# Performance work log

Hardware: AMD Instinct MI355X
Metric: run time of the kernel (lower is better)

Reference implementation:

```python
import math
import jax, jax.numpy as jnp
import numpy as np
from jax.scipy.special import gammaln, xlogy

HEADS = 8
DIM_KEY = 64
DIM_VALUE = 64
NUM_REL_POS_FEATURES = 192
DIM = 768
SEQ = 2048
BATCH = 2


def get_positional_embed(seq_len: int, feature_size: int) -> jnp.ndarray:
    # distances: [2n-1]
    distances = jnp.arange(-seq_len + 1, seq_len, dtype=jnp.float32)
    f = feature_size // 6  # 3 basis classes, then doubled with sign term
    absd = jnp.abs(distances)[:, None]  # [2n-1, 1]
    # exponential basis
    max_range = math.log(seq_len) / math.log(2.0)
    half_life = 2.0 ** jnp.linspace(3.0, max_range, f)[None, :]
    exp_feat = jnp.exp(-math.log(2.0) / half_life * absd)
    # central mask basis
    center_widths = 2.0 ** jnp.arange(1, f + 1, dtype=jnp.float32) - 1.0
    cmask = (center_widths[None, :] > absd).astype(jnp.float32)
    # gamma pdf basis
    stddev = seq_len / (2.0 * f)
    start_mean = seq_len / f
    mean = jnp.linspace(start_mean, float(seq_len), f)[None, :]
    concentration = (mean / stddev) ** 2
    rate = mean / stddev ** 2
    log_unnorm = xlogy(concentration - 1.0, absd) - rate * absd
    log_norm = gammaln(concentration) - concentration * jnp.log(rate)
    probs = jnp.exp(log_unnorm - log_norm) + 1e-8
    gamma_feat = probs / jnp.max(probs, axis=-1, keepdims=True)
    emb = jnp.concatenate([exp_feat, cmask, gamma_feat], axis=-1)  # [2n-1, 3f]
    return jnp.concatenate([emb, jnp.sign(distances)[:, None] * emb], axis=-1)  # [2n-1, 6f]


def relative_shift(x: jnp.ndarray) -> jnp.ndarray:
    # x: [b, h, n, 2n-1] -> [b, h, n, n] via Transformer-XL shift trick
    x = jnp.concatenate([jnp.zeros_like(x[..., :1]), x], axis=-1)
    b, h, t1, t2 = x.shape  # t2 = 2n
    x = x.reshape(b, h, t2, t1)[:, :, 1:, :].reshape(b, h, t1, t2 - 1)
    return x[..., : (t2 + 1) // 2]


def setup_inputs() -> dict:
    key = jax.random.key(0)
    ks = jax.random.split(key, 9)
    d_inner = HEADS * DIM_KEY
    d_vinner = HEADS * DIM_VALUE
    sc = 1.0 / math.sqrt(DIM)
    return {
        "x": jax.random.normal(ks[0], (BATCH, SEQ, DIM), dtype=jnp.float32),
        "Wq": jax.random.normal(ks[1], (DIM, d_inner), dtype=jnp.float32) * sc,
        "Wk": jax.random.normal(ks[2], (DIM, d_inner), dtype=jnp.float32) * sc,
        "Wv": jax.random.normal(ks[3], (DIM, d_vinner), dtype=jnp.float32) * sc,
        "Wrel": jax.random.normal(ks[4], (NUM_REL_POS_FEATURES, d_inner), dtype=jnp.float32) * (1.0 / math.sqrt(NUM_REL_POS_FEATURES)),
        "rel_content_bias": jax.random.normal(ks[5], (1, HEADS, 1, DIM_KEY), dtype=jnp.float32),
        "rel_pos_bias": jax.random.normal(ks[6], (1, HEADS, 1, DIM_KEY), dtype=jnp.float32),
        "Wo": jax.random.normal(ks[7], (d_vinner, DIM), dtype=jnp.float32) * (1.0 / math.sqrt(d_vinner)),
        "bo": jax.random.normal(ks[8], (DIM,), dtype=jnp.float32) * 0.01,
    }


def reference(x, Wq, Wk, Wv, Wrel, rel_content_bias, rel_pos_bias, Wo, bo):
    b, n, _ = x.shape
    scale = DIM_KEY ** -0.5
    # projections -> [b, h, n, d]
    q = (x @ Wq).reshape(b, n, HEADS, DIM_KEY).transpose(0, 2, 1, 3) * scale
    k = (x @ Wk).reshape(b, n, HEADS, DIM_KEY).transpose(0, 2, 1, 3)
    v = (x @ Wv).reshape(b, n, HEADS, DIM_VALUE).transpose(0, 2, 1, 3)
    content_logits = jnp.einsum("bhid,bhjd->bhij", q + rel_content_bias, k)
    positions = get_positional_embed(n, NUM_REL_POS_FEATURES)  # [2n-1, F]
    rel_k = (positions @ Wrel).reshape(2 * n - 1, HEADS, DIM_KEY).transpose(1, 0, 2)  # [h, 2n-1, d]
    rel_logits = jnp.einsum("bhid,hjd->bhij", q + rel_pos_bias, rel_k)
    rel_logits = relative_shift(rel_logits)  # [b, h, n, n]
    attn = jax.nn.softmax(content_logits + rel_logits, axis=-1)
    out = jnp.einsum("bhij,bhjd->bhid", attn, v)  # [b, h, n, dv]
    out = out.transpose(0, 2, 1, 3).reshape(b, n, HEADS * DIM_VALUE)
    return out @ Wo + bo
```

## Files before the change

kernel.cpp:

```cpp
#include <hip/hip_runtime.h>
#include <hip/hip_bf16.h>
#include <math.h>


typedef _Float16 f16x8 __attribute__((ext_vector_type(8)));
typedef _Float16 f16x4 __attribute__((ext_vector_type(4)));
typedef float f32x4 __attribute__((ext_vector_type(4)));

#define MFMA16(a, b, c) __builtin_amdgcn_mfma_f32_16x16x32_f16((a), (b), (c), 0, 0, 0)

__global__ __launch_bounds__(256) void cvt4_kernel(const float* __restrict__ in,
                                                   _Float16* __restrict__ out, int n4) {
  int idx = blockIdx.x * 256 + threadIdx.x;
  if (idx < n4) {
    float4 v = ((const float4*)in)[idx];
    f16x4 o;
    o[0] = (_Float16)v.x; o[1] = (_Float16)v.y; o[2] = (_Float16)v.z; o[3] = (_Float16)v.w;
    ((f16x4*)out)[idx] = o;
  }
}

__global__ __launch_bounds__(256) void cvt_t_tile_kernel(const float* __restrict__ in,
                                                         _Float16* __restrict__ out,
                                                         int K, int N) {
  __shared__ float tile[32][33];
  const int k0 = blockIdx.y * 32, n0 = blockIdx.x * 32;
  const int t = threadIdx.x;
  const int tr = t >> 3, tc = (t & 7) * 4;
  float4 v = *(const float4*)(in + (size_t)(k0 + tr) * N + n0 + tc);
  tile[tr][tc] = v.x; tile[tr][tc + 1] = v.y; tile[tr][tc + 2] = v.z; tile[tr][tc + 3] = v.w;
  __syncthreads();
  f16x4 o;
  o[0] = (_Float16)tile[tc][tr];
  o[1] = (_Float16)tile[tc + 1][tr];
  o[2] = (_Float16)tile[tc + 2][tr];
  o[3] = (_Float16)tile[tc + 3][tr];
  *(f16x4*)(out + (size_t)(n0 + tr) * K + k0 + tc) = o;
}

__global__ __launch_bounds__(256) void cvt_t3_tile_kernel(const float* __restrict__ Wq,
                                                          const float* __restrict__ Wk,
                                                          const float* __restrict__ Wv,
                                                          _Float16* __restrict__ out) {
  __shared__ float tile[32][33];
  const int z = blockIdx.z;
  const float* in = (z == 0) ? Wq : (z == 1) ? Wk : Wv;
  const int k0 = blockIdx.y * 32, n0 = blockIdx.x * 32;
  const int t = threadIdx.x;
  const int tr = t >> 3, tc = (t & 7) * 4;
  float4 v = *(const float4*)(in + (size_t)(k0 + tr) * 512 + n0 + tc);
  tile[tr][tc] = v.x; tile[tr][tc + 1] = v.y; tile[tr][tc + 2] = v.z; tile[tr][tc + 3] = v.w;
  __syncthreads();
  f16x4 o;
  o[0] = (_Float16)tile[tc][tr];
  o[1] = (_Float16)tile[tc + 1][tr];
  o[2] = (_Float16)tile[tc + 2][tr];
  o[3] = (_Float16)tile[tc + 3][tr];
  *(f16x4*)(out + ((size_t)z * 512 + n0 + tr) * 768 + k0 + tc) = o;
}

__global__ __launch_bounds__(64) void pos_const_kernel(float* __restrict__ lnrm) {
  int t = threadIdx.x;
  if (t < 32) {
    float mean = 64.f * (float)(t + 1);
    float sd = 32.f;
    float conc = (mean / sd) * (mean / sd);
    float rate = mean / (sd * sd);
    lnrm[t] = lgammaf(conc) - conc * logf(rate);
  }
}

__global__ __launch_bounds__(128) void pos_embed_kernel(_Float16* __restrict__ posb,
                                                        const float* __restrict__ lnrm) {
  const int t = threadIdx.x;
  const int lr = t >> 5, i = t & 31;
  const int r = blockIdx.x * 4 + lr;
  _Float16* row = posb + (size_t)r * 192;
  if (r >= 4095) {
    row[i] = (_Float16)0.f; row[32 + i] = (_Float16)0.f; row[64 + i] = (_Float16)0.f;
    row[96 + i] = (_Float16)0.f; row[128 + i] = (_Float16)0.f; row[160 + i] = (_Float16)0.f;
    return;
  }
  const float dist = (float)(r - 2047);
  const float absd = fabsf(dist);
  const float sgn = (dist > 0.f) ? 1.f : ((dist < 0.f) ? -1.f : 0.f);
  const float e = 3.f + (float)i * (8.f / 31.f);
  const float expv = exp2f(-absd * exp2f(-e));
  const float cw = exp2f((float)(i + 1)) - 1.f;
  const float cm = (cw > absd) ? 1.f : 0.f;
  const float mean = 64.f * (float)(i + 1);
  const float conc = (mean / 32.f) * (mean / 32.f);
  const float rate = mean / 1024.f;
  const float lu = (conc - 1.f) * logf(absd) - rate * absd;
  float gv = expf(lu - lnrm[i]) + 1e-8f;
  float mx = gv;
  mx = fmaxf(mx, __shfl_xor(mx, 1));
  mx = fmaxf(mx, __shfl_xor(mx, 2));
  mx = fmaxf(mx, __shfl_xor(mx, 4));
  mx = fmaxf(mx, __shfl_xor(mx, 8));
  mx = fmaxf(mx, __shfl_xor(mx, 16));
  gv /= mx;
  row[i] = (_Float16)expv;       row[32 + i] = (_Float16)cm;        row[64 + i] = (_Float16)gv;
  row[96 + i] = (_Float16)(sgn * expv); row[128 + i] = (_Float16)(sgn * cm); row[160 + i] = (_Float16)(sgn * gv);
}

template <int MODE>
__global__ __launch_bounds__(256, 3) void gemm_tile(
    const _Float16* __restrict__ A, const _Float16* __restrict__ Bt,
    const int N, const int K,
    _Float16* __restrict__ o0, _Float16* __restrict__ o1,
    _Float16* __restrict__ o2, _Float16* __restrict__ o3,
    const float* __restrict__ bias0, const float* __restrict__ bias1,
    float* __restrict__ outf) {
  __shared__ __align__(16) _Float16 As[2][128 * 32];
  __shared__ __align__(16) _Float16 Bs[2][128 * 32];
  const int tid = threadIdx.x;
  const int w = tid >> 6, lane = tid & 63, g = lane >> 4, m = lane & 15;
  const int wr = w >> 1, wc = w & 1;
  const int row0 = blockIdx.y * 128;
  const int c0 = blockIdx.x * 128;

  const int sr0 = tid >> 2, ssl = tid & 3;
  const _Float16* Ag = A + (size_t)(row0 + sr0) * K + ssl * 8;
  const _Float16* Bg = Bt + (size_t)(c0 + sr0) * K + ssl * 8;
  const size_t gstep = (size_t)64 * K;
  const int wo0 = sr0 * 64 + ((ssl ^ ((sr0 >> 1) & 3)) << 4);

  int aoff[4], boff[4];
#pragma unroll
  for (int i = 0; i < 4; ++i) {
    const int ar = wr * 64 + i * 16 + m;
    aoff[i] = ar * 64 + ((g ^ ((ar >> 1) & 3)) << 4);
    const int br = wc * 64 + i * 16 + m;
    boff[i] = br * 64 + ((g ^ ((br >> 1) & 3)) << 4);
  }

  f16x8 a0, a1, b0, b1;
#define GLOAD(k0v)                                      \
  a0 = *(const f16x8*)(Ag + (k0v));                     \
  a1 = *(const f16x8*)(Ag + gstep + (k0v));             \
  b0 = *(const f16x8*)(Bg + (k0v));                     \
  b1 = *(const f16x8*)(Bg + gstep + (k0v));
#define SWRITE(buf)                                     \
  *(f16x8*)((char*)As[buf] + wo0) = a0;                 \
  *(f16x8*)((char*)As[buf] + wo0 + 4096) = a1;          \
  *(f16x8*)((char*)Bs[buf] + wo0) = b0;                 \
  *(f16x8*)((char*)Bs[buf] + wo0 + 4096) = b1;

  f32x4 acc[4][4] = {};
  GLOAD(0); SWRITE(0);
  __syncthreads();
  const int nk = K >> 5;
  for (int ks = 0; ks < nk; ++ks) {
    const int cur = ks & 1;
    if (ks + 1 < nk) { GLOAD((ks + 1) << 5); }
    const char* ap = (const char*)As[cur];
    const char* bp = (const char*)Bs[cur];
    f16x8 af[4], bf[4];
#pragma unroll
    for (int i = 0; i < 4; ++i) {
      af[i] = *(const f16x8*)(ap + aoff[i]);
      bf[i] = *(const f16x8*)(bp + boff[i]);
    }
#pragma unroll
    for (int mi = 0; mi < 4; ++mi)
#pragma unroll
      for (int ni = 0; ni < 4; ++ni)
        acc[mi][ni] = MFMA16(af[mi], bf[ni], acc[mi][ni]);
    if (ks + 1 < nk) { SWRITE(cur ^ 1); }
    __syncthreads();
  }
#undef GLOAD
#undef SWRITE

  const int proj = (MODE == 0) ? (c0 >> 9) : 0;
#pragma unroll
  for (int ni = 0; ni < 4; ++ni) {
    const int col = c0 + wc * 64 + ni * 16 + m;
    const int c = col & 511, hh = (MODE == 0) ? (c >> 6) : (col >> 6);
    const int dk = col & 63;
    float b0f = 0.f, b1f = 0.f;
    if (MODE == 0 && proj == 0) { b0f = bias0[c]; b1f = bias1[c]; }
    if (MODE == 0 && proj == 2) {
#pragma unroll
      for (int mi = 0; mi < 4; ++mi) {
        const int rowb = row0 + wr * 64 + mi * 16 + g * 4;
        const int bb = rowb >> 11, n = rowb & 2047;
        f16x4 pk;
#pragma unroll
        for (int r = 0; r < 4; ++r) pk[r] = (_Float16)acc[mi][ni][r];
        *(f16x4*)(o3 + ((size_t)(bb * 8 + hh) * 64 + dk) * 2048 + n) = pk;
      }
    } else {
#pragma unroll
      for (int mi = 0; mi < 4; ++mi) {
#pragma unroll
        for (int r = 0; r < 4; ++r) {
          const int row = row0 + wr * 64 + mi * 16 + g * 4 + r;
          const float v = acc[mi][ni][r];
          if (MODE == 0) {
            const int bb = row >> 11, n = row & 2047;
            const size_t ad = ((size_t)(bb * 8 + hh) * 2048 + n) * 64 + dk;
            if (proj == 0) {
              const float vs = v * 0.125f;
              o0[ad] = (_Float16)(vs + b0f);
              o1[ad] = (_Float16)(vs + b1f);
            } else {
              o2[ad] = (_Float16)v;
            }
          } else if (MODE == 3) {
            o0[((size_t)hh * 4096 + row) * 64 + dk] = (_Float16)v;
          } else {
            outf[(size_t)row * N + col] = v + bias0[col];
          }
        }
      }
    }
  }
}

__global__ __launch_bounds__(256, 2) void attn_kernel(
    const _Float16* __restrict__ qc, const _Float16* __restrict__ qp,
    const _Float16* __restrict__ kb, const _Float16* __restrict__ vtb,
    const _Float16* __restrict__ relkb, _Float16* __restrict__ attnb) {
  __shared__ __align__(16) char lds[2 * 32768 + 4 * 2304];
  const int tid = threadIdx.x;
  const int w = tid >> 6, lane = tid & 63, g = lane >> 4, m = lane & 15;
  const int L = blockIdx.x;
  const int h = L & 7;
  const int r2 = L >> 3;
  const int b = r2 >> 5, xt = r2 & 31;
  const int bh = b * 8 + h;
  const int i0b = xt << 6;
  const int i0 = i0b + w * 16;

  const int srow = tid >> 3;
  const int ssl = tid & 7;
  const int swz = (srow << 7) + ((ssl ^ (srow & 7)) << 4);
  const char* kgb = (const char*)kb + ((size_t)bh << 18);
  const char* vgb = (const char*)vtb + ((size_t)bh << 18);
  const char* rgb = (const char*)relkb + ((size_t)h << 19);

  f16x8 ska, skb_, sva, svb, sra, srb, src_, srd;
#define STAGE_LOAD(j0v, d0v)                                                          \
  ska  = *(const f16x8*)(kgb + ((size_t)((j0v) + srow) << 7) + (ssl << 4));           \
  skb_ = *(const f16x8*)(kgb + ((size_t)((j0v) + srow + 32) << 7) + (ssl << 4));      \
  sva  = *(const f16x8*)(vgb + ((size_t)srow << 12) + ((j0v) << 1) + (ssl << 4));     \
  svb  = *(const f16x8*)(vgb + ((size_t)(srow + 32) << 12) + ((j0v) << 1) + (ssl << 4)); \
  sra  = *(const f16x8*)(rgb + ((size_t)((d0v) + srow) << 7) + (ssl << 4));           \
  srb  = *(const f16x8*)(rgb + ((size_t)((d0v) + srow + 32) << 7) + (ssl << 4));      \
  src_ = *(const f16x8*)(rgb + ((size_t)((d0v) + srow + 64) << 7) + (ssl << 4));      \
  srd  = *(const f16x8*)(rgb + ((size_t)((d0v) + srow + 96) << 7) + (ssl << 4));

#define STAGE_WRITE(halfp)                          \
  *(f16x8*)((halfp) + swz) = ska;                   \
  *(f16x8*)((halfp) + swz + 4096) = skb_;           \
  *(f16x8*)((halfp) + 8192 + swz) = sva;            \
  *(f16x8*)((halfp) + 8192 + swz + 4096) = svb;     \
  *(f16x8*)((halfp) + 16384 + swz) = sra;           \
  *(f16x8*)((halfp) + 16384 + swz + 4096) = srb;    \
  *(f16x8*)((halfp) + 16384 + swz + 8192) = src_;   \
  *(f16x8*)((halfp) + 16384 + swz + 12288) = srd;

  STAGE_LOAD(0, 1984 - i0b);
  { char* nh = lds; STAGE_WRITE(nh); }

  const size_t qbase = ((size_t)bh * 2048 + i0 + m) * 64 + g * 8;
  f16x8 qcf0 = *(const f16x8*)(qc + qbase);
  f16x8 qcf1 = *(const f16x8*)(qc + qbase + 32);
  f16x8 qpf0 = *(const f16x8*)(qp + qbase);
  f16x8 qpf1 = *(const f16x8*)(qp + qbase + 32);

  __syncthreads();

  f32x4 acc_o[4] = {};
  float m_run[4], l_run[4];
#pragma unroll
  for (int r = 0; r < 4; ++r) { m_run[r] = -1e30f; l_run[r] = 0.f; }

  const int sx = m & 7;
  const int fo0 = (g ^ sx) << 4;
  const int fo1 = ((4 | g) ^ sx) << 4;
  const int rrow0 = 48 - (w << 4) + m;
  _Float16* Pl = (_Float16*)(lds + 65536 + w * 2304);

  for (int jt = 0; jt < 32; ++jt) {
    if (jt < 31) {
      const int j0n = (jt + 1) << 6;
      STAGE_LOAD(j0n, j0n - i0b + 1984);
    }
    const char* curh = lds + ((jt & 1) << 15);
    f32x4 sc[4] = {};
#pragma unroll
    for (int cf = 0; cf < 4; ++cf) {
      const char* kp = curh + ((m + (cf << 4)) << 7);
      sc[cf] = MFMA16(qcf0, *(const f16x8*)(kp + fo0), sc[cf]);
      sc[cf] = MFMA16(qcf1, *(const f16x8*)(kp + fo1), sc[cf]);
    }
    f32x4 rc[5] = {};
#pragma unroll
    for (int cf = 0; cf < 5; ++cf) {
      const char* rp = curh + 16384 + ((rrow0 + (cf << 4)) << 7);
      rc[cf] = MFMA16(qpf0, *(const f16x8*)(rp + fo0), rc[cf]);
      rc[cf] = MFMA16(qpf1, *(const f16x8*)(rp + fo1), rc[cf]);
    }
#pragma unroll
    for (int r = 0; r < 4; ++r) {
      const int lr = g * 4 + r;
      const int u = 15 + m - lr;
      const int src = (g << 4) | (u & 15);
      const bool hi = (m > lr);
      float sh0 = __shfl(rc[0][r], src);
      float sh1 = __shfl(rc[1][r], src);
      float sh2 = __shfl(rc[2][r], src);
      float sh3 = __shfl(rc[3][r], src);
      float sh4 = __shfl(rc[4][r], src);
      sc[0][r] += hi ? sh1 : sh0;
      sc[1][r] += hi ? sh2 : sh1;
      sc[2][r] += hi ? sh3 : sh2;
      sc[3][r] += hi ? sh4 : sh3;
    }
    float P[4][4];
#pragma unroll
    for (int r = 0; r < 4; ++r) {
      float mx = fmaxf(fmaxf(sc[0][r], sc[1][r]), fmaxf(sc[2][r], sc[3][r]));
      mx = fmaxf(mx, __shfl_xor(mx, 1));
      mx = fmaxf(mx, __shfl_xor(mx, 2));
      mx = fmaxf(mx, __shfl_xor(mx, 4));
      mx = fmaxf(mx, __shfl_xor(mx, 8));
      const float mnew = fmaxf(m_run[r], mx);
      const float corr = __expf(m_run[r] - mnew);
      float rs = 0.f;
#pragma unroll
      for (int cf = 0; cf < 4; ++cf) {
        float p = __expf(sc[cf][r] - mnew);
        P[cf][r] = p;
        rs += p;
      }
      rs += __shfl_xor(rs, 1);
      rs += __shfl_xor(rs, 2);
      rs += __shfl_xor(rs, 4);
      rs += __shfl_xor(rs, 8);
      l_run[r] = l_run[r] * corr + rs;
      m_run[r] = mnew;
#pragma unroll
      for (int cf = 0; cf < 4; ++cf) acc_o[cf][r] *= corr;
    }
#pragma unroll
    for (int cf = 0; cf < 4; ++cf)
#pragma unroll
      for (int r = 0; r < 4; ++r)
        Pl[(g * 4 + r) * 72 + cf * 16 + m] = (_Float16)P[cf][r];
#pragma unroll
    for (int ks = 0; ks < 2; ++ks) {
      f16x8 pa = *(const f16x8*)((const char*)Pl + m * 144 + ks * 64 + (g << 4));
#pragma unroll
      for (int cf = 0; cf < 4; ++cf) {
        const char* vp = curh + 8192 + ((m + (cf << 4)) << 7);
        acc_o[cf] = MFMA16(pa, *(const f16x8*)(vp + (ks ? fo1 : fo0)), acc_o[cf]);
      }
    }
    if (jt < 31) {
      char* nh = lds + (((jt & 1) ^ 1) << 15);
      STAGE_WRITE(nh);
    }
    __syncthreads();
  }
#pragma unroll
  for (int cf = 0; cf < 4; ++cf)
#pragma unroll
    for (int r = 0; r < 4; ++r) {
      const int i = i0 + g * 4 + r;
      const float o = acc_o[cf][r] / l_run[r];
      attnb[((size_t)(b * 2048 + i)) * 512 + h * 64 + cf * 16 + m] = (_Float16)o;
    }
#undef STAGE_LOAD
#undef STAGE_WRITE
}

extern "C" void kernel_launch(void* const* d_in, const int* in_sizes, int n_in,
                              void* d_out, int out_size, void* d_ws, size_t ws_size,
                              hipStream_t stream) {
  (void)in_sizes; (void)n_in; (void)out_size; (void)ws_size;
  const float* x    = (const float*)d_in[0];
  const float* Wq   = (const float*)d_in[1];
  const float* Wk   = (const float*)d_in[2];
  const float* Wv   = (const float*)d_in[3];
  const float* Wrel = (const float*)d_in[4];
  const float* bc   = (const float*)d_in[5];
  const float* bp   = (const float*)d_in[6];
  const float* Wo   = (const float*)d_in[7];
  const float* bo   = (const float*)d_in[8];
  float* out = (float*)d_out;

  char* ws = (char*)d_ws;
  size_t off = 0;
  auto alloc = [&](size_t bytes) -> void* {
    void* p = ws + off;
    off += (bytes + 255) & ~(size_t)255;
    return p;
  };
  _Float16* xb     = (_Float16*)alloc(4096ull * 768 * 2);
  _Float16* wqkvt  = (_Float16*)alloc(1536ull * 768 * 2);
  _Float16* wrelt  = (_Float16*)alloc(512ull * 192 * 2);
  _Float16* wot    = (_Float16*)alloc(768ull * 512 * 2);
  _Float16* posb   = (_Float16*)alloc(4096ull * 192 * 2);
  float*    lnrm   = (float*)alloc(32 * 4);
  _Float16* qcb    = (_Float16*)alloc(16ull * 2048 * 64 * 2);
  _Float16* qpb    = (_Float16*)alloc(16ull * 2048 * 64 * 2);
  _Float16* kbb    = (_Float16*)alloc(16ull * 2048 * 64 * 2);
  _Float16* vtb    = (_Float16*)alloc(16ull * 64 * 2048 * 2);
  _Float16* relkb  = (_Float16*)alloc(8ull * 4096 * 64 * 2);
  _Float16* attnb  = (_Float16*)alloc(4096ull * 512 * 2);

  cvt4_kernel<<<3072, 256, 0, stream>>>(x, xb, 786432);
  cvt_t3_tile_kernel<<<dim3(16, 24, 3), 256, 0, stream>>>(Wq, Wk, Wv, wqkvt);
  cvt_t_tile_kernel<<<dim3(16, 6), 256, 0, stream>>>(Wrel, wrelt, 192, 512);
  cvt_t_tile_kernel<<<dim3(24, 16), 256, 0, stream>>>(Wo, wot, 512, 768);
  pos_const_kernel<<<1, 64, 0, stream>>>(lnrm);
  pos_embed_kernel<<<1024, 128, 0, stream>>>(posb, lnrm);

  gemm_tile<0><<<dim3(12, 32), 256, 0, stream>>>(xb, wqkvt, 1536, 768,
                                                 qcb, qpb, kbb, vtb, bc, bp, nullptr);
  gemm_tile<3><<<dim3(4, 32), 256, 0, stream>>>(posb, wrelt, 512, 192,
                                                relkb, nullptr, nullptr, nullptr,
                                                nullptr, nullptr, nullptr);

  attn_kernel<<<512, 256, 0, stream>>>(qcb, qpb, kbb, vtb, relkb, attnb);

  gemm_tile<4><<<dim3(6, 32), 256, 0, stream>>>(attnb, wot, 768, 512,
                                                nullptr, nullptr, nullptr, nullptr,
                                                bo, nullptr, out);
}
```

Measured before the change: 213.5 us.

## Fuse prep kernels, use direct global-to-LDS loads, shrink GEMM tiles, MFMA row sums

All conversion and positional-embedding kernels are merged into one prep launch, and the lgamma constants are computed inline. The GEMM and attention kernels now stage K/V/rel-K and GEMM operands with global_load_lds, which copies straight into shared memory without passing through registers. The swizzle moves to the global source address. GEMM tiles shrink to 64 rows with occupancy 4 and twice the grid to fill more CUs. In attention, the softmax max reduction uses DPP and the row sum is accumulated by an MFMA against a ones vector instead of shuffles, which adds some MFMA work.

```diff
diff --git a/kernel.cpp b/kernel.cpp
--- a/kernel.cpp
+++ b/kernel.cpp
@@ -9,72 +9,75 @@
 
 #define MFMA16(a, b, c) __builtin_amdgcn_mfma_f32_16x16x32_f16((a), (b), (c), 0, 0, 0)
 
-__global__ __launch_bounds__(256) void cvt4_kernel(const float* __restrict__ in,
-                                                   _Float16* __restrict__ out, int n4) {
-  int idx = blockIdx.x * 256 + threadIdx.x;
-  if (idx < n4) {
-    float4 v = ((const float4*)in)[idx];
+#define GL16(gp, lp)                                                       \
+  __builtin_amdgcn_global_load_lds(                                        \
+      (const __attribute__((address_space(1))) void*)(gp),                 \
+      (__attribute__((address_space(3))) void*)(lp), 16, 0, 0)
+
+__device__ __forceinline__ float dpp_fmax16(float x) {
+  int v;
+  v = __builtin_amdgcn_update_dpp(0, __float_as_int(x), 0xB1, 0xf, 0xf, true);
+  x = fmaxf(x, __int_as_float(v));
+  v = __builtin_amdgcn_update_dpp(0, __float_as_int(x), 0x4E, 0xf, 0xf, true);
+  x = fmaxf(x, __int_as_float(v));
+  v = __builtin_amdgcn_update_dpp(0, __float_as_int(x), 0x141, 0xf, 0xf, true);
+  x = fmaxf(x, __int_as_float(v));
+  v = __builtin_amdgcn_update_dpp(0, __float_as_int(x), 0x140, 0xf, 0xf, true);
+  x = fmaxf(x, __int_as_float(v));
+  return x;
+}
+
+__global__ __launch_bounds__(256) void prep_kernel(
+    const float* __restrict__ x, const float* __restrict__ Wq,
+    const float* __restrict__ Wk, const float* __restrict__ Wv,
+    const float* __restrict__ Wrel, const float* __restrict__ Wo,
+    _Float16* __restrict__ xb, _Float16* __restrict__ wqkvt,
+    _Float16* __restrict__ wrelt, _Float16* __restrict__ wot,
+    _Float16* __restrict__ posb) {
+  __shared__ float tile[32][33];
+  const int t = threadIdx.x;
+  int bid = blockIdx.x;
+  if (bid < 3072) {
+    const int idx = bid * 256 + t;
+    float4 v = ((const float4*)x)[idx];
     f16x4 o;
     o[0] = (_Float16)v.x; o[1] = (_Float16)v.y; o[2] = (_Float16)v.z; o[3] = (_Float16)v.w;
-    ((f16x4*)out)[idx] = o;
-  }
-}
-
-__global__ __launch_bounds__(256) void cvt_t_tile_kernel(const float* __restrict__ in,
-                                                         _Float16* __restrict__ out,
-                                                         int K, int N) {
-  __shared__ float tile[32][33];
-  const int k0 = blockIdx.y * 32, n0 = blockIdx.x * 32;
-  const int t = threadIdx.x;
-  const int tr = t >> 3, tc = (t & 7) * 4;
-  float4 v = *(const float4*)(in + (size_t)(k0 + tr) * N + n0 + tc);
-  tile[tr][tc] = v.x; tile[tr][tc + 1] = v.y; tile[tr][tc + 2] = v.z; tile[tr][tc + 3] = v.w;
-  __syncthreads();
-  f16x4 o;
-  o[0] = (_Float16)tile[tc][tr];
-  o[1] = (_Float16)tile[tc + 1][tr];
-  o[2] = (_Float16)tile[tc + 2][tr];
-  o[3] = (_Float16)tile[tc + 3][tr];
-  *(f16x4*)(out + (size_t)(n0 + tr) * K + k0 + tc) = o;
-}
-
-__global__ __launch_bounds__(256) void cvt_t3_tile_kernel(const float* __restrict__ Wq,
-                                                          const float* __restrict__ Wk,
-                                                          const float* __restrict__ Wv,
-                                                          _Float16* __restrict__ out) {
-  __shared__ float tile[32][33];
-  const int z = blockIdx.z;
-  const float* in = (z == 0) ? Wq : (z == 1) ? Wk : Wv;
-  const int k0 = blockIdx.y * 32, n0 = blockIdx.x * 32;
-  const int t = threadIdx.x;
-  const int tr = t >> 3, tc = (t & 7) * 4;
-  float4 v = *(const float4*)(in + (size_t)(k0 + tr) * 512 + n0 + tc);
-  tile[tr][tc] = v.x; tile[tr][tc + 1] = v.y; tile[tr][tc + 2] = v.z; tile[tr][tc + 3] = v.w;
-  __syncthreads();
-  f16x4 o;
-  o[0] = (_Float16)tile[tc][tr];
-  o[1] = (_Float16)tile[tc + 1][tr];
-  o[2] = (_Float16)tile[tc + 2][tr];
-  o[3] = (_Float16)tile[tc + 3][tr];
-  *(f16x4*)(out + ((size_t)z * 512 + n0 + tr) * 768 + k0 + tc) = o;
-}
-
-__global__ __launch_bounds__(64) void pos_const_kernel(float* __restrict__ lnrm) {
-  int t = threadIdx.x;
-  if (t < 32) {
-    float mean = 64.f * (float)(t + 1);
-    float sd = 32.f;
-    float conc = (mean / sd) * (mean / sd);
-    float rate = mean / (sd * sd);
-    lnrm[t] = lgammaf(conc) - conc * logf(rate);
-  }
-}
-
-__global__ __launch_bounds__(128) void pos_embed_kernel(_Float16* __restrict__ posb,
-                                                        const float* __restrict__ lnrm) {
-  const int t = threadIdx.x;
+    ((f16x4*)xb)[idx] = o;
+    return;
+  }
+  bid -= 3072;
+  if (bid < 1632) {
+    const float* in; _Float16* out; int K_, N_, bx, by;
+    if (bid < 1152) {
+      const int z = bid / 384, rem = bid % 384;
+      in = (z == 0) ? Wq : (z == 1) ? Wk : Wv;
+      out = wqkvt + (size_t)z * 512 * 768;
+      K_ = 768; N_ = 512; bx = rem & 15; by = rem >> 4;
+    } else if (bid < 1248) {
+      const int rem = bid - 1152;
+      in = Wrel; out = wrelt;
+      K_ = 192; N_ = 512; bx = rem & 15; by = rem >> 4;
+    } else {
+      const int rem = bid - 1248;
+      in = Wo; out = wot;
+      K_ = 512; N_ = 768; bx = rem % 24; by = rem / 24;
+    }
+    const int k0 = by * 32, n0 = bx * 32;
+    const int tr = t >> 3, tc = (t & 7) * 4;
+    float4 v = *(const float4*)(in + (size_t)(k0 + tr) * N_ + n0 + tc);
+    tile[tr][tc] = v.x; tile[tr][tc + 1] = v.y; tile[tr][tc + 2] = v.z; tile[tr][tc + 3] = v.w;
+    __syncthreads();
+    f16x4 o;
+    o[0] = (_Float16)tile[tc][tr];
+    o[1] = (_Float16)tile[tc + 1][tr];
+    o[2] = (_Float16)tile[tc + 2][tr];
+    o[3] = (_Float16)tile[tc + 3][tr];
+    *(f16x4*)(out + (size_t)(n0 + tr) * K_ + k0 + tc) = o;
+    return;
+  }
+  bid -= 1632;
   const int lr = t >> 5, i = t & 31;
-  const int r = blockIdx.x * 4 + lr;
+  const int r = bid * 8 + lr;
   _Float16* row = posb + (size_t)r * 192;
   if (r >= 4095) {
     row[i] = (_Float16)0.f; row[32 + i] = (_Float16)0.f; row[64 + i] = (_Float16)0.f;
@@ -91,8 +94,9 @@
   const float mean = 64.f * (float)(i + 1);
   const float conc = (mean / 32.f) * (mean / 32.f);
   const float rate = mean / 1024.f;
+  const float lnrm = lgammaf(conc) - conc * logf(rate);
   const float lu = (conc - 1.f) * logf(absd) - rate * absd;
-  float gv = expf(lu - lnrm[i]) + 1e-8f;
+  float gv = expf(lu - lnrm) + 1e-8f;
   float mx = gv;
   mx = fmaxf(mx, __shfl_xor(mx, 1));
   mx = fmaxf(mx, __shfl_xor(mx, 2));
@@ -100,78 +104,76 @@
   mx = fmaxf(mx, __shfl_xor(mx, 8));
   mx = fmaxf(mx, __shfl_xor(mx, 16));
   gv /= mx;
-  row[i] = (_Float16)expv;       row[32 + i] = (_Float16)cm;        row[64 + i] = (_Float16)gv;
-  row[96 + i] = (_Float16)(sgn * expv); row[128 + i] = (_Float16)(sgn * cm); row[160 + i] = (_Float16)(sgn * gv);
+  row[i] = (_Float16)expv;              row[32 + i] = (_Float16)cm;
+  row[64 + i] = (_Float16)gv;           row[96 + i] = (_Float16)(sgn * expv);
+  row[128 + i] = (_Float16)(sgn * cm);  row[160 + i] = (_Float16)(sgn * gv);
 }
 
 template <int MODE>
-__global__ __launch_bounds__(256, 3) void gemm_tile(
+__global__ __launch_bounds__(256, 4) void gemm_tile(
     const _Float16* __restrict__ A, const _Float16* __restrict__ Bt,
     const int N, const int K,
     _Float16* __restrict__ o0, _Float16* __restrict__ o1,
     _Float16* __restrict__ o2, _Float16* __restrict__ o3,
     const float* __restrict__ bias0, const float* __restrict__ bias1,
     float* __restrict__ outf) {
-  __shared__ __align__(16) _Float16 As[2][128 * 32];
+  __shared__ __align__(16) _Float16 As[2][64 * 32];
   __shared__ __align__(16) _Float16 Bs[2][128 * 32];
   const int tid = threadIdx.x;
   const int w = tid >> 6, lane = tid & 63, g = lane >> 4, m = lane & 15;
   const int wr = w >> 1, wc = w & 1;
-  const int row0 = blockIdx.y * 128;
+  const int row0 = blockIdx.y * 64;
   const int c0 = blockIdx.x * 128;
 
-  const int sr0 = tid >> 2, ssl = tid & 3;
-  const _Float16* Ag = A + (size_t)(row0 + sr0) * K + ssl * 8;
-  const _Float16* Bg = Bt + (size_t)(c0 + sr0) * K + ssl * 8;
-  const size_t gstep = (size_t)64 * K;
-  const int wo0 = sr0 * 64 + ((ssl ^ ((sr0 >> 1) & 3)) << 4);
-
-  int aoff[4], boff[4];
+  const int arow = tid >> 2, asl = tid & 3;
+  const int axor = asl ^ ((arow >> 1) & 3);
+  const char* Ag = (const char*)(A + (size_t)(row0 + arow) * K) + (axor << 4);
+  const int adst = (arow << 6) + (asl << 4);
+  const int brow = w * 32 + (lane >> 2);
+  const int bxor = asl ^ ((brow >> 1) & 3);
+  const char* Bg = (const char*)(Bt + (size_t)(c0 + brow) * K) + (bxor << 4);
+  const size_t bstep = (size_t)16 * K * 2;
+  const int bdst = (brow << 6) + (asl << 4);
+
+  int aoff[2], boff[4];
+#pragma unroll
+  for (int i = 0; i < 2; ++i) {
+    const int ar = wr * 32 + i * 16 + m;
+    aoff[i] = (ar << 6) + ((g ^ ((ar >> 1) & 3)) << 4);
+  }
 #pragma unroll
   for (int i = 0; i < 4; ++i) {
-    const int ar = wr * 64 + i * 16 + m;
-    aoff[i] = ar * 64 + ((g ^ ((ar >> 1) & 3)) << 4);
     const int br = wc * 64 + i * 16 + m;
-    boff[i] = br * 64 + ((g ^ ((br >> 1) & 3)) << 4);
-  }
-
-  f16x8 a0, a1, b0, b1;
-#define GLOAD(k0v)                                      \
-  a0 = *(const f16x8*)(Ag + (k0v));                     \
-  a1 = *(const f16x8*)(Ag + gstep + (k0v));             \
-  b0 = *(const f16x8*)(Bg + (k0v));                     \
-  b1 = *(const f16x8*)(Bg + gstep + (k0v));
-#define SWRITE(buf)                                     \
-  *(f16x8*)((char*)As[buf] + wo0) = a0;                 \
-  *(f16x8*)((char*)As[buf] + wo0 + 4096) = a1;          \
-  *(f16x8*)((char*)Bs[buf] + wo0) = b0;                 \
-  *(f16x8*)((char*)Bs[buf] + wo0 + 4096) = b1;
-
-  f32x4 acc[4][4] = {};
-  GLOAD(0); SWRITE(0);
+    boff[i] = (br << 6) + ((g ^ ((br >> 1) & 3)) << 4);
+  }
+
+#define STAGEG(buf, k0v)                                       \
+  GL16(Ag + ((k0v) << 1), (char*)As[buf] + adst);              \
+  GL16(Bg + ((k0v) << 1), (char*)Bs[buf] + bdst);              \
+  GL16(Bg + bstep + ((k0v) << 1), (char*)Bs[buf] + bdst + 1024);
+
+  f32x4 acc[2][4] = {};
+  STAGEG(0, 0);
   __syncthreads();
   const int nk = K >> 5;
   for (int ks = 0; ks < nk; ++ks) {
     const int cur = ks & 1;
-    if (ks + 1 < nk) { GLOAD((ks + 1) << 5); }
+    if (ks + 1 < nk) { STAGEG(cur ^ 1, (ks + 1) << 5); }
     const char* ap = (const char*)As[cur];
     const char* bp = (const char*)Bs[cur];
-    f16x8 af[4], bf[4];
-#pragma unroll
-    for (int i = 0; i < 4; ++i) {
-      af[i] = *(const f16x8*)(ap + aoff[i]);
-      bf[i] = *(const f16x8*)(bp + boff[i]);
-    }
-#pragma unroll
-    for (int mi = 0; mi < 4; ++mi)
+    f16x8 af[2], bf[4];
+#pragma unroll
+    for (int i = 0; i < 2; ++i) af[i] = *(const f16x8*)(ap + aoff[i]);
+#pragma unroll
+    for (int i = 0; i < 4; ++i) bf[i] = *(const f16x8*)(bp + boff[i]);
+#pragma unroll
+    for (int mi = 0; mi < 2; ++mi)
 #pragma unroll
       for (int ni = 0; ni < 4; ++ni)
         acc[mi][ni] = MFMA16(af[mi], bf[ni], acc[mi][ni]);
-    if (ks + 1 < nk) { SWRITE(cur ^ 1); }
     __syncthreads();
   }
-#undef GLOAD
-#undef SWRITE
+#undef STAGEG
 
   const int proj = (MODE == 0) ? (c0 >> 9) : 0;
 #pragma unroll
@@ -183,8 +185,8 @@
     if (MODE == 0 && proj == 0) { b0f = bias0[c]; b1f = bias1[c]; }
     if (MODE == 0 && proj == 2) {
 #pragma unroll
-      for (int mi = 0; mi < 4; ++mi) {
-        const int rowb = row0 + wr * 64 + mi * 16 + g * 4;
+      for (int mi = 0; mi < 2; ++mi) {
+        const int rowb = row0 + wr * 32 + mi * 16 + g * 4;
         const int bb = rowb >> 11, n = rowb & 2047;
         f16x4 pk;
 #pragma unroll
@@ -193,10 +195,10 @@
       }
     } else {
 #pragma unroll
-      for (int mi = 0; mi < 4; ++mi) {
+      for (int mi = 0; mi < 2; ++mi) {
 #pragma unroll
         for (int r = 0; r < 4; ++r) {
-          const int row = row0 + wr * 64 + mi * 16 + g * 4 + r;
+          const int row = row0 + wr * 32 + mi * 16 + g * 4 + r;
           const float v = acc[mi][ni][r];
           if (MODE == 0) {
             const int bb = row >> 11, n = row & 2047;
@@ -234,36 +236,24 @@
   const int i0b = xt << 6;
   const int i0 = i0b + w * 16;
 
-  const int srow = tid >> 3;
-  const int ssl = tid & 7;
-  const int swz = (srow << 7) + ((ssl ^ (srow & 7)) << 4);
-  const char* kgb = (const char*)kb + ((size_t)bh << 18);
-  const char* vgb = (const char*)vtb + ((size_t)bh << 18);
-  const char* rgb = (const char*)relkb + ((size_t)h << 19);
-
-  f16x8 ska, skb_, sva, svb, sra, srb, src_, srd;
-#define STAGE_LOAD(j0v, d0v)                                                          \
-  ska  = *(const f16x8*)(kgb + ((size_t)((j0v) + srow) << 7) + (ssl << 4));           \
-  skb_ = *(const f16x8*)(kgb + ((size_t)((j0v) + srow + 32) << 7) + (ssl << 4));      \
-  sva  = *(const f16x8*)(vgb + ((size_t)srow << 12) + ((j0v) << 1) + (ssl << 4));     \
-  svb  = *(const f16x8*)(vgb + ((size_t)(srow + 32) << 12) + ((j0v) << 1) + (ssl << 4)); \
-  sra  = *(const f16x8*)(rgb + ((size_t)((d0v) + srow) << 7) + (ssl << 4));           \
-  srb  = *(const f16x8*)(rgb + ((size_t)((d0v) + srow + 32) << 7) + (ssl << 4));      \
-  src_ = *(const f16x8*)(rgb + ((size_t)((d0v) + srow + 64) << 7) + (ssl << 4));      \
-  srd  = *(const f16x8*)(rgb + ((size_t)((d0v) + srow + 96) << 7) + (ssl << 4));
-
-#define STAGE_WRITE(halfp)                          \
-  *(f16x8*)((halfp) + swz) = ska;                   \
-  *(f16x8*)((halfp) + swz + 4096) = skb_;           \
-  *(f16x8*)((halfp) + 8192 + swz) = sva;            \
-  *(f16x8*)((halfp) + 8192 + swz + 4096) = svb;     \
-  *(f16x8*)((halfp) + 16384 + swz) = sra;           \
-  *(f16x8*)((halfp) + 16384 + swz + 4096) = srb;    \
-  *(f16x8*)((halfp) + 16384 + swz + 8192) = src_;   \
-  *(f16x8*)((halfp) + 16384 + swz + 12288) = srd;
-
-  STAGE_LOAD(0, 1984 - i0b);
-  { char* nh = lds; STAGE_WRITE(nh); }
+  const int srow = tid >> 3, ssl = tid & 7;
+  const int sxr16 = (ssl ^ (srow & 7)) << 4;
+  const int dst16 = (srow << 7) + (ssl << 4);
+  const char* kgs = (const char*)kb + ((size_t)bh << 18) + sxr16;
+  const char* vgs = (const char*)vtb + ((size_t)bh << 18) + ((size_t)srow << 12) + sxr16;
+  const char* rgs = (const char*)relkb + ((size_t)h << 19) + sxr16;
+
+#define STAGE(halfp, j0v, d0v)                                                  \
+  GL16(kgs + ((size_t)((j0v) + srow) << 7), (halfp) + dst16);                   \
+  GL16(kgs + ((size_t)((j0v) + srow + 32) << 7), (halfp) + dst16 + 4096);       \
+  GL16(vgs + ((j0v) << 1), (halfp) + 8192 + dst16);                             \
+  GL16(vgs + ((size_t)32 << 12) + ((j0v) << 1), (halfp) + 8192 + dst16 + 4096); \
+  GL16(rgs + ((size_t)((d0v) + srow) << 7), (halfp) + 16384 + dst16);           \
+  GL16(rgs + ((size_t)((d0v) + srow + 32) << 7), (halfp) + 16384 + dst16 + 4096); \
+  GL16(rgs + ((size_t)((d0v) + srow + 64) << 7), (halfp) + 16384 + dst16 + 8192); \
+  GL16(rgs + ((size_t)((d0v) + srow + 96) << 7), (halfp) + 16384 + dst16 + 12288);
+
+  STAGE(lds, 0, 1984 - i0b);
 
   const size_t qbase = ((size_t)bh * 2048 + i0 + m) * 64 + g * 8;
   f16x8 qcf0 = *(const f16x8*)(qc + qbase);
@@ -271,12 +261,17 @@
   f16x8 qpf0 = *(const f16x8*)(qp + qbase);
   f16x8 qpf1 = *(const f16x8*)(qp + qbase + 32);
 
+  f16x8 onesv;
+#pragma unroll
+  for (int i = 0; i < 8; ++i) onesv[i] = (_Float16)1.f;
+
   __syncthreads();
 
   f32x4 acc_o[4] = {};
-  float m_run[4], l_run[4];
-#pragma unroll
-  for (int r = 0; r < 4; ++r) { m_run[r] = -1e30f; l_run[r] = 0.f; }
+  f32x4 acc_l = {};
+  float m_run[4];
+#pragma unroll
+  for (int r = 0; r < 4; ++r) m_run[r] = -1e30f;
 
   const int sx = m & 7;
   const int fo0 = (g ^ sx) << 4;
@@ -287,7 +282,8 @@
   for (int jt = 0; jt < 32; ++jt) {
     if (jt < 31) {
       const int j0n = (jt + 1) << 6;
-      STAGE_LOAD(j0n, j0n - i0b + 1984);
+      char* nh = lds + (((jt & 1) ^ 1) << 15);
+      STAGE(nh, j0n, j0n - i0b + 1984);
     }
     const char* curh = lds + ((jt & 1) << 15);
     f32x4 sc[4] = {};
@@ -324,27 +320,16 @@
 #pragma unroll
     for (int r = 0; r < 4; ++r) {
       float mx = fmaxf(fmaxf(sc[0][r], sc[1][r]), fmaxf(sc[2][r], sc[3][r]));
-      mx = fmaxf(mx, __shfl_xor(mx, 1));
-      mx = fmaxf(mx, __shfl_xor(mx, 2));
-      mx = fmaxf(mx, __shfl_xor(mx, 4));
-      mx = fmaxf(mx, __shfl_xor(mx, 8));
+      mx = dpp_fmax16(mx);
       const float mnew = fmaxf(m_run[r], mx);
       const float corr = __expf(m_run[r] - mnew);
-      float rs = 0.f;
+      m_run[r] = mnew;
 #pragma unroll
       for (int cf = 0; cf < 4; ++cf) {
-        float p = __expf(sc[cf][r] - mnew);
-        P[cf][r] = p;
-        rs += p;
+        P[cf][r] = __expf(sc[cf][r] - mnew);
+        acc_o[cf][r] *= corr;
       }
-      rs += __shfl_xor(rs, 1);
-      rs += __shfl_xor(rs, 2);
-      rs += __shfl_xor(rs, 4);
-      rs += __shfl_xor(rs, 8);
-      l_run[r] = l_run[r] * corr + rs;
-      m_run[r] = mnew;
-#pragma unroll
-      for (int cf = 0; cf < 4; ++cf) acc_o[cf][r] *= corr;
+      acc_l[r] *= corr;
     }
 #pragma unroll
     for (int cf = 0; cf < 4; ++cf)
@@ -359,10 +344,7 @@
         const char* vp = curh + 8192 + ((m + (cf << 4)) << 7);
         acc_o[cf] = MFMA16(pa, *(const f16x8*)(vp + (ks ? fo1 : fo0)), acc_o[cf]);
       }
-    }
-    if (jt < 31) {
-      char* nh = lds + (((jt & 1) ^ 1) << 15);
-      STAGE_WRITE(nh);
+      acc_l = MFMA16(pa, onesv, acc_l);
     }
     __syncthreads();
   }
@@ -371,11 +353,10 @@
 #pragma unroll
     for (int r = 0; r < 4; ++r) {
       const int i = i0 + g * 4 + r;
-      const float o = acc_o[cf][r] / l_run[r];
+      const float o = acc_o[cf][r] / acc_l[r];
       attnb[((size_t)(b * 2048 + i)) * 512 + h * 64 + cf * 16 + m] = (_Float16)o;
     }
-#undef STAGE_LOAD
-#undef STAGE_WRITE
+#undef STAGE
 }
 
 extern "C" void kernel_launch(void* const* d_in, const int* in_sizes, int n_in,
@@ -405,7 +386,6 @@
   _Float16* wrelt  = (_Float16*)alloc(512ull * 192 * 2);
   _Float16* wot    = (_Float16*)alloc(768ull * 512 * 2);
   _Float16* posb   = (_Float16*)alloc(4096ull * 192 * 2);
-  float*    lnrm   = (float*)alloc(32 * 4);
   _Float16* qcb    = (_Float16*)alloc(16ull * 2048 * 64 * 2);
   _Float16* qpb    = (_Float16*)alloc(16ull * 2048 * 64 * 2);
   _Float16* kbb    = (_Float16*)alloc(16ull * 2048 * 64 * 2);
@@ -413,22 +393,18 @@
   _Float16* relkb  = (_Float16*)alloc(8ull * 4096 * 64 * 2);
   _Float16* attnb  = (_Float16*)alloc(4096ull * 512 * 2);
 
-  cvt4_kernel<<<3072, 256, 0, stream>>>(x, xb, 786432);
-  cvt_t3_tile_kernel<<<dim3(16, 24, 3), 256, 0, stream>>>(Wq, Wk, Wv, wqkvt);
-  cvt_t_tile_kernel<<<dim3(16, 6), 256, 0, stream>>>(Wrel, wrelt, 192, 512);
-  cvt_t_tile_kernel<<<dim3(24, 16), 256, 0, stream>>>(Wo, wot, 512, 768);
-  pos_const_kernel<<<1, 64, 0, stream>>>(lnrm);
-  pos_embed_kernel<<<1024, 128, 0, stream>>>(posb, lnrm);
-
-  gemm_tile<0><<<dim3(12, 32), 256, 0, stream>>>(xb, wqkvt, 1536, 768,
+  prep_kernel<<<5216, 256, 0, stream>>>(x, Wq, Wk, Wv, Wrel, Wo,
+                                        xb, wqkvt, wrelt, wot, posb);
+
+  gemm_tile<0><<<dim3(12, 64), 256, 0, stream>>>(xb, wqkvt, 1536, 768,
                                                  qcb, qpb, kbb, vtb, bc, bp, nullptr);
-  gemm_tile<3><<<dim3(4, 32), 256, 0, stream>>>(posb, wrelt, 512, 192,
+  gemm_tile<3><<<dim3(4, 64), 256, 0, stream>>>(posb, wrelt, 512, 192,
                                                 relkb, nullptr, nullptr, nullptr,
                                                 nullptr, nullptr, nullptr);
 
   attn_kernel<<<512, 256, 0, stream>>>(qcb, qpb, kbb, vtb, relkb, attnb);
 
-  gemm_tile<4><<<dim3(6, 32), 256, 0, stream>>>(attnb, wot, 768, 512,
+  gemm_tile<4><<<dim3(6, 64), 256, 0, stream>>>(attnb, wot, 768, 512,
                                                 nullptr, nullptr, nullptr, nullptr,
                                                 bo, nullptr, out);
 }
```

New measurement: 191.5 us. 1.11x faster.
